# Kernel optimization log

Hardware: AMD Instinct MI355X
Metric: run time of the kernel (lower is better)

The kernel has to match this reference:

```python
import jax, jax.numpy as jnp
import numpy as np

HS, NH, HD = 768, 12, 64
MLP_DIM = 3072
WS = 14            # window size
B, H, W = 8, 64, 64
EPS = 1e-6


def _ln(x, g, b):
    mu = jnp.mean(x, axis=-1, keepdims=True)
    var = jnp.mean(jnp.square(x - mu), axis=-1, keepdims=True)
    return (x - mu) * jax.lax.rsqrt(var + EPS) * g + b


def setup_inputs() -> dict:
    key = jax.random.key(0)
    ks = jax.random.split(key, 8)
    s = 0.02
    return {
        "x": jax.random.normal(ks[0], (B, H, W, HS), dtype=jnp.float32),
        "ln1_g": jnp.ones((HS,), jnp.float32),
        "ln1_b": jnp.zeros((HS,), jnp.float32),
        "qkv_w": jax.random.normal(ks[1], (HS, 3 * HS), jnp.float32) * s,
        "qkv_b": jnp.zeros((3 * HS,), jnp.float32),
        "proj_w": jax.random.normal(ks[2], (HS, HS), jnp.float32) * s,
        "proj_b": jnp.zeros((HS,), jnp.float32),
        "rel_pos_h": jax.random.normal(ks[3], (2 * WS - 1, HD), jnp.float32) * s,
        "rel_pos_w": jax.random.normal(ks[4], (2 * WS - 1, HD), jnp.float32) * s,
        "ln2_g": jnp.ones((HS,), jnp.float32),
        "ln2_b": jnp.zeros((HS,), jnp.float32),
        "mlp_w1": jax.random.normal(ks[5], (HS, MLP_DIM), jnp.float32) * s,
        "mlp_b1": jnp.zeros((MLP_DIM,), jnp.float32),
        "mlp_w2": jax.random.normal(ks[6], (MLP_DIM, HS), jnp.float32) * s,
        "mlp_b2": jnp.zeros((HS,), jnp.float32),
    }


def reference(x, ln1_g, ln1_b, qkv_w, qkv_b, proj_w, proj_b,
              rel_pos_h, rel_pos_w, ln2_g, ln2_b,
              mlp_w1, mlp_b1, mlp_w2, mlp_b2):
    b, h, w, c = x.shape
    shortcut = x
    y = _ln(x, ln1_g, ln1_b)

    # ---- window partition (pad H,W to multiple of WS) ----
    pad = (-h) % WS
    hp = h + pad
    y = jnp.pad(y, ((0, 0), (0, pad), (0, pad), (0, 0)))
    n = hp // WS  # windows per side
    y = y.reshape(b, n, WS, n, WS, c).transpose(0, 1, 3, 2, 4, 5)
    y = y.reshape(b * n * n, WS, WS, c)          # (Bw, 14, 14, C)
    bw = y.shape[0]
    tok = WS * WS                                 # 196

    # ---- attention with decomposed relative position bias ----
    qkv = y.reshape(bw, tok, c) @ qkv_w + qkv_b   # (Bw, 196, 3C)
    qkv = qkv.reshape(bw, tok, 3, NH, HD).transpose(2, 0, 3, 1, 4)
    qkv = qkv.reshape(3, bw * NH, tok, HD)
    q, k, v = qkv[0], qkv[1], qkv[2]
    scale = HD ** -0.5
    attn = jnp.einsum('bqd,bkd->bqk', q * scale, k)  # (Bw*NH, 196, 196)

    idx = jnp.arange(WS)[:, None] - jnp.arange(WS)[None, :] + (WS - 1)
    Rh = rel_pos_h[idx]                            # (14, 14, HD)
    Rw = rel_pos_w[idx]                            # (14, 14, HD)
    qr = q.reshape(bw * NH, WS, WS, HD)
    rel_h = jnp.einsum('bhwc,hkc->bhwk', qr, Rh)   # (Bnh, h, w, k_h)
    rel_w = jnp.einsum('bhwc,wkc->bhwk', qr, Rw)   # (Bnh, h, w, k_w)
    bias = (rel_h[:, :, :, :, None] + rel_w[:, :, :, None, :])
    attn = attn + bias.reshape(bw * NH, tok, tok)

    attn = jax.nn.softmax(attn, axis=-1)
    out = jnp.einsum('bqk,bkd->bqd', attn, v)      # (Bw*NH, 196, HD)
    out = out.reshape(bw, NH, WS, WS, HD).transpose(0, 2, 3, 1, 4)
    out = out.reshape(bw, WS, WS, c) @ proj_w + proj_b

    # ---- window unpartition + crop ----
    out = out.reshape(b, n, n, WS, WS, c).transpose(0, 1, 3, 2, 4, 5)
    out = out.reshape(b, hp, hp, c)[:, :h, :w, :]

    x = shortcut + out

    # ---- MLP block ----
    y2 = _ln(x, ln2_g, ln2_b)
    y2 = jax.nn.gelu(y2 @ mlp_w1 + mlp_b1, approximate=False) @ mlp_w2 + mlp_b2
    return x + y2
```

## Files before the change

### kernel.cpp

```cpp
#include <hip/hip_runtime.h>
#include <hip/hip_bf16.h>
#include <math.h>


#define HS 768
#define NHEADS 12
#define HD 64
#define WSZ 14
#define TOK 196
#define HWDIM 64
#define NSIDE 5
#define WIN_PER_B 25

typedef __attribute__((ext_vector_type(8))) short short8;
typedef __attribute__((ext_vector_type(4))) float floatx4;
typedef __attribute__((ext_vector_type(4))) unsigned short ushort4v;

__device__ __forceinline__ float bf2f(unsigned short u) {
    union { unsigned int i; float f; } w; w.i = ((unsigned int)u) << 16; return w.f;
}
__device__ __forceinline__ unsigned short f2bu(float f) {
    __hip_bfloat16 h = __float2bfloat16(f);
    return *(unsigned short*)&h;
}

__device__ __forceinline__ void gload16(const void* g, void* l) {
    __builtin_amdgcn_global_load_lds(
        (const __attribute__((address_space(1))) void*)g,
        (__attribute__((address_space(3))) void*)l, 16, 0, 0);
}

__device__ __forceinline__ int gather_src(int m, int M, int win_base) {
    if (m >= M) return -1;
    int lwin = m / TOK, tok = m - lwin * TOK;
    int win = win_base + lwin;
    int bb = win / WIN_PER_B, r = win - bb * WIN_PER_B;
    int wi = r / NSIDE, wj = r - wi * NSIDE;
    int ti = tok / WSZ, tj = tok - ti * WSZ;
    int h = wi * WSZ + ti, w = wj * WSZ + tj;
    if (h < HWDIM && w < HWDIM) return (bb * HWDIM + h) * HWDIM + w;
    return -1;
}

__global__ __launch_bounds__(256)
void cvt_t_k(const float* __restrict__ src, __hip_bfloat16* __restrict__ dst,
             int K, int N) {
    __shared__ float t[32][33];
    int n0 = blockIdx.x * 32, k0 = blockIdx.y * 32;
    int tc = threadIdx.x & 31, tr8 = threadIdx.x >> 5;
    #pragma unroll
    for (int i = 0; i < 4; ++i) {
        int r = tr8 + i * 8;
        t[r][tc] = src[(size_t)(k0 + r) * N + n0 + tc];
    }
    __syncthreads();
    #pragma unroll
    for (int i = 0; i < 4; ++i) {
        int r = tr8 + i * 8;
        dst[(size_t)(n0 + r) * K + k0 + tc] = __float2bfloat16(t[tc][r]);
    }
}

__global__ __launch_bounds__(256)
void ln_k(const float* __restrict__ x, const float* __restrict__ g,
          const float* __restrict__ b, __hip_bfloat16* __restrict__ y) {
    int wave = threadIdx.x >> 6, lane = threadIdx.x & 63;
    int row = blockIdx.x * 4 + wave;
    const float4* xr = (const float4*)(x + (size_t)row * HS);
    float4 a0 = xr[lane], a1 = xr[lane + 64], a2 = xr[lane + 128];
    float s = a0.x + a0.y + a0.z + a0.w + a1.x + a1.y + a1.z + a1.w
            + a2.x + a2.y + a2.z + a2.w;
    float q = a0.x*a0.x + a0.y*a0.y + a0.z*a0.z + a0.w*a0.w
            + a1.x*a1.x + a1.y*a1.y + a1.z*a1.z + a1.w*a1.w
            + a2.x*a2.x + a2.y*a2.y + a2.z*a2.z + a2.w*a2.w;
    #pragma unroll
    for (int off = 32; off > 0; off >>= 1) {
        s += __shfl_down(s, off, 64);
        q += __shfl_down(q, off, 64);
    }
    s = __shfl(s, 0, 64);
    q = __shfl(q, 0, 64);
    float mu = s * (1.0f / HS);
    float var = q * (1.0f / HS) - mu * mu;
    float rstd = rsqrtf(var + 1e-6f);
    const float4* g4 = (const float4*)g;
    const float4* b4 = (const float4*)b;
    unsigned short* yr = (unsigned short*)y + (size_t)row * HS;
    float4 av[3] = {a0, a1, a2};
    #pragma unroll
    for (int c = 0; c < 3; ++c) {
        float4 gv = g4[lane + 64 * c], bv = b4[lane + 64 * c];
        float4 a = av[c];
        ushort4v o;
        o[0] = f2bu((a.x - mu) * rstd * gv.x + bv.x);
        o[1] = f2bu((a.y - mu) * rstd * gv.y + bv.y);
        o[2] = f2bu((a.z - mu) * rstd * gv.z + bv.z);
        o[3] = f2bu((a.w - mu) * rstd * gv.w + bv.w);
        *(ushort4v*)&yr[(lane + 64 * c) * 4] = o;
    }
}

template<int EP, int AGATHER, int BM, int BN, int KSPLIT, int XSWZ = 0, int RING = 3>
__global__ __launch_bounds__(256, 4)
void gemm_k(const __hip_bfloat16* __restrict__ A,
            const __hip_bfloat16* __restrict__ Bt,
            const float* __restrict__ bias,
            int M, int N, int K,
            __hip_bfloat16* __restrict__ oq, __hip_bfloat16* __restrict__ okk,
            __hip_bfloat16* __restrict__ ov,
            float* __restrict__ of, const float* __restrict__ resid,
            __hip_bfloat16* __restrict__ oh,
            int win_base, int m_base)
{
    constexpr int LPW = (BM + BN) / 64;
    constexpr int FI = BM / 32;
    constexpr int FJ = BN / 32;
    constexpr int ASZ = BM * 32;
    constexpr int BSZ = BN * 32;
    __shared__ __align__(16) unsigned short lds[RING * (ASZ + BSZ)];
    unsigned short* Asb = lds;
    unsigned short* Bsb = lds + RING * ASZ;

    int tid = threadIdx.x;
    int wave = tid >> 6, lane = tid & 63;
    int n16 = lane & 15, quad = lane >> 4;
    int wrr = wave >> 1, wcc = wave & 1;

    int bx = blockIdx.x, by = blockIdx.y;
    if constexpr (XSWZ) {
        int gx = gridDim.x, gy = gridDim.y;
        int lin = by * gx + bx;
        int nwg = gx * gy;
        int qq = nwg >> 3, rr8 = nwg & 7;
        int xcd = lin & 7, pos = lin >> 3;
        int swz = (xcd < rr8) ? (xcd * (qq + 1) + pos)
                              : (rr8 * (qq + 1) + (xcd - rr8) * qq + pos);
        bx = swz % gx;
        by = swz / gx;
    }
    int bm = by * BM;
    int bn = bx * BN;
    int kz = (KSPLIT > 1) ? blockIdx.z : 0;
    int kseg = K / KSPLIT;

    int srow = tid >> 2;
    int q4 = tid & 3;
    int skoff = (q4 ^ ((srow >> 1) & 3)) << 3;

    const unsigned short* Au = (const unsigned short*)A;
    const unsigned short* Bu = (const unsigned short*)Bt;

    int src0 = 0, src1 = 0;
    if (AGATHER) {
        int s0 = gather_src(bm + srow, M, win_base);
        src0 = s0 >= 0 ? s0 : 0;
        if (BM == 128) {
            int s1 = gather_src(bm + 64 + srow, M, win_base);
            src1 = s1 >= 0 ? s1 : 0;
        }
    } else {
        int m0 = bm + srow;
        src0 = m0 < M ? m0 : 0;
        if (BM == 128) { int m1 = bm + 64 + srow; src1 = m1 < M ? m1 : 0; }
    }

    const unsigned short* ap0 = Au + (size_t)src0 * K + kz * kseg + skoff;
    const unsigned short* ap1 = Au + (size_t)src1 * K + kz * kseg + skoff;
    const unsigned short* bp0 = Bu + (size_t)(bn + srow) * K + kz * kseg + skoff;
    const unsigned short* bp1 = Bu + (size_t)(bn + 64 + srow) * K + kz * kseg + skoff;

    auto stage = [&](int kt, int b) {
        size_t ko = (size_t)kt * 32;
        gload16(ap0 + ko, Asb + b * ASZ + wave * 512);
        if constexpr (BM == 128) gload16(ap1 + ko, Asb + b * ASZ + 2048 + wave * 512);
        gload16(bp0 + ko, Bsb + b * BSZ + wave * 512);
        if constexpr (BN == 128) gload16(bp1 + ko, Bsb + b * BSZ + 2048 + wave * 512);
    };

    floatx4 acc[FI][FJ] = {};
    int xr = (n16 >> 1) & 3;
    int nt = kseg >> 5;

    stage(0, 0);
    if (nt > 1) stage(1, 1);
    if (RING > 3 && nt > 2) stage(2, 2);

    int cur = 0;
    for (int t = 0; t < nt; ++t) {
        int ahead = nt - 1 - t;
        if (RING >= 4 && ahead >= 2) {
            if constexpr (LPW == 4)      asm volatile("s_waitcnt vmcnt(8)" ::: "memory");
            else if constexpr (LPW == 3) asm volatile("s_waitcnt vmcnt(6)" ::: "memory");
            else                         asm volatile("s_waitcnt vmcnt(4)" ::: "memory");
        } else if (ahead >= 1) {
            if constexpr (LPW == 4)      asm volatile("s_waitcnt vmcnt(4)" ::: "memory");
            else if constexpr (LPW == 3) asm volatile("s_waitcnt vmcnt(3)" ::: "memory");
            else                         asm volatile("s_waitcnt vmcnt(2)" ::: "memory");
        } else {
            asm volatile("s_waitcnt vmcnt(0)" ::: "memory");
        }
        __builtin_amdgcn_s_barrier();
        if (t + RING - 1 < nt) {
            int nb = cur + RING - 1; if (nb >= RING) nb -= RING;
            stage(t + RING - 1, nb);
        }
        short8 af[FI], bf[FJ];
        #pragma unroll
        for (int i = 0; i < FI; ++i) {
            int ra = wrr * (BM / 2) + i * 16 + n16;
            af[i] = *(const short8*)&Asb[cur * ASZ + ra * 32 + ((quad ^ xr) << 3)];
        }
        #pragma unroll
        for (int j = 0; j < FJ; ++j) {
            int rb = wcc * (BN / 2) + j * 16 + n16;
            bf[j] = *(const short8*)&Bsb[cur * BSZ + rb * 32 + ((quad ^ xr) << 3)];
        }
        #pragma unroll
        for (int i = 0; i < FI; ++i)
            #pragma unroll
            for (int j = 0; j < FJ; ++j)
                acc[i][j] = __builtin_amdgcn_mfma_f32_16x16x32_bf16(
                    af[i], bf[j], acc[i][j], 0, 0, 0);
        asm volatile("s_waitcnt lgkmcnt(0)" ::: "memory");
        cur += 1; if (cur >= RING) cur -= RING;
    }

    int rbase = bm + wrr * (BM / 2) + quad * 4;
    int cbase = bn + wcc * (BN / 2) + n16;

    if constexpr (EP == 0 || EP == 2) {
        constexpr int CLD = BN + 8;
        __syncthreads();
        unsigned short* Cs = lds;
        int ruseW[FI * 4];
        if (EP == 0) {
            #pragma unroll
            for (int i = 0; i < FI; ++i)
                #pragma unroll
                for (int r = 0; r < 4; ++r)
                    ruseW[i * 4 + r] = gather_src(rbase + i * 16 + r, M, win_base) >= 0;
        }
        #pragma unroll
        for (int j = 0; j < FJ; ++j) {
            int col_l = wcc * (BN / 2) + j * 16 + n16;
            float bcol = bias[bn + col_l];
            #pragma unroll
            for (int i = 0; i < FI; ++i) {
                #pragma unroll
                for (int r = 0; r < 4; ++r) {
                    int row_l = wrr * (BM / 2) + i * 16 + quad * 4 + r;
                    float val = acc[i][j][r] + bcol;
                    float vv;
                    if (EP == 0) {
                        vv = ruseW[i * 4 + r] ? val : bcol;
                    } else {
                        vv = 0.5f * val * (1.0f + erff(val * 0.70710678118654752f));
                    }
                    Cs[row_l * CLD + col_l] = f2bu(vv);
                }
            }
        }
        __syncthreads();
        #pragma unroll
        for (int rep = 0; rep < (BM * (BN / 64)) / 256; ++rep) {
            int idx = rep * 256 + tid;
            int row_l = idx / (BN / 64);
            int half = idx - row_l * (BN / 64);
            int m = bm + row_l;
            if (m < M) {
                unsigned short* srcu = &Cs[row_l * CLD + half * 64];
                unsigned short* dstu;
                if (EP == 0) {
                    int lwin = m / TOK, tok = m - lwin * TOK;
                    int colg = bn + half * 64;
                    int which = colg / HS;
                    int head = (colg - which * HS) >> 6;
                    __hip_bfloat16* dstp = (which == 0) ? oq : ((which == 1) ? okk : ov);
                    dstu = (unsigned short*)dstp +
                           ((size_t)(lwin * NHEADS + head) * TOK + tok) * HD;
                } else {
                    dstu = (unsigned short*)oh + (size_t)m * N + bn + half * 64;
                }
                #pragma unroll
                for (int s = 0; s < 8; ++s)
                    *(uint4*)(dstu + s * 8) = *(const uint4*)(srcu + s * 8);
            }
        }
    } else {
        int rowoff[FI * 4];
        int ruse[FI * 4];
        #pragma unroll
        for (int i = 0; i < FI; ++i) {
            #pragma unroll
            for (int r = 0; r < 4; ++r) {
                int ii = i * 4 + r;
                int row = rbase + i * 16 + r;
                if (EP == 1) {
                    int lwin = row / TOK, tok = row - lwin * TOK;
                    int win = win_base + lwin;
                    int bb = win / WIN_PER_B, rr2 = win - bb * WIN_PER_B;
                    int wi = rr2 / NSIDE, wj = rr2 - wi * NSIDE;
                    int ti = tok / WSZ, tj = tok - ti * WSZ;
                    int h = wi * WSZ + ti, w = wj * WSZ + tj;
                    ruse[ii] = (h < HWDIM) && (w < HWDIM);
                    rowoff[ii] = ((bb * HWDIM + h) * HWDIM + w) * HS;
                } else {
                    rowoff[ii] = (m_base + row) * HS;
                    ruse[ii] = 1;
                }
            }
        }
        #pragma unroll
        for (int j = 0; j < FJ; ++j) {
            int col = cbase + j * 16;
            float bcol = bias[col];
            if (EP == 3 && KSPLIT > 1 && kz != 0) bcol = 0.0f;
            #pragma unroll
            for (int i = 0; i < FI; ++i) {
                #pragma unroll
                for (int r = 0; r < 4; ++r) {
                    int ii = i * 4 + r;
                    int row = rbase + i * 16 + r;
                    if (row >= M) continue;
                    float val = acc[i][j][r] + bcol;
                    if (EP == 1) {
                        if (ruse[ii]) {
                            size_t idx = (size_t)rowoff[ii] + col;
                            of[idx] = resid[idx] + val;
                        }
                    } else {
                        size_t idx = (size_t)rowoff[ii] + col;
                        if (KSPLIT > 1) {
                            unsafeAtomicAdd(&of[idx], val);
                        } else {
                            of[idx] += val;
                        }
                    }
                }
            }
        }
    }
}

__global__ __launch_bounds__(256)
void attn_k(const __hip_bfloat16* __restrict__ qb, const __hip_bfloat16* __restrict__ kb,
            const __hip_bfloat16* __restrict__ vb,
            const float* __restrict__ rph, const float* __restrict__ rpw,
            __hip_bfloat16* __restrict__ ao)
{
    __shared__ __align__(16) unsigned short lds[40736];
    unsigned short* Ks = lds;
    unsigned short* Vt = lds + 14112;
    unsigned short* KE = lds + 28960;
    unsigned short* scr = lds + 37280;

    int bid = blockIdx.x;
    int lwin = bid / NHEADS, head = bid - lwin * NHEADS;
    size_t base = (size_t)(lwin * NHEADS + head) * TOK * HD;
    const unsigned short* q = (const unsigned short*)qb + base;
    const unsigned short* k = (const unsigned short*)kb + base;
    const unsigned short* v = (const unsigned short*)vb + base;

    int tid = threadIdx.x;
    int wave = tid >> 6, lane = tid & 63;
    int n16 = lane & 15, quad = lane >> 4;

    short8 btab[4][2];
    #pragma unroll
    for (int nt = 0; nt < 4; ++nt) {
        int n = nt * 16 + n16;
        #pragma unroll
        for (int kh = 0; kh < 2; ++kh) {
            short8 f = {0, 0, 0, 0, 0, 0, 0, 0};
            if (n < 54) {
                const float* src = (n < 27) ? (rph + (size_t)n * HD)
                                            : (rpw + (size_t)(n - 27) * HD);
                const float4* s4 = (const float4*)(src + kh * 32 + quad * 8);
                float4 a = s4[0], b = s4[1];
                f[0] = (short)f2bu(a.x * 8.0f); f[1] = (short)f2bu(a.y * 8.0f);
                f[2] = (short)f2bu(a.z * 8.0f); f[3] = (short)f2bu(a.w * 8.0f);
                f[4] = (short)f2bu(b.x * 8.0f); f[5] = (short)f2bu(b.y * 8.0f);
                f[6] = (short)f2bu(b.z * 8.0f); f[7] = (short)f2bu(b.w * 8.0f);
            }
            btab[nt][kh] = f;
        }
    }

    for (int idx = tid; idx < 1568; idx += 256) {
        int row = idx >> 3, q8 = (idx & 7) << 3;
        *(uint4*)&Ks[row * 72 + q8] = *(const uint4*)(k + (size_t)row * HD + q8);
    }
    for (int s = tid; s < 1568; s += 256) {
        int row = s >> 3, d8 = (s & 7) << 3;
        uint4 vv = *(const uint4*)(v + (size_t)row * HD + d8);
        const unsigned short* p = (const unsigned short*)&vv;
        #pragma unroll
        for (int e = 0; e < 8; ++e)
            Vt[(d8 + e) * 232 + row] = p[e];
    }
    for (int s = tid; s < 64 * 9; s += 256) {
        int r = s / 9, c = 196 + (s - r * 9) * 4;
        uint2 z = {0u, 0u};
        *(uint2*)&Vt[r * 232 + c] = z;
    }
    for (int krow = tid; krow < 208; krow += 256) {
        int ki = krow / WSZ, kj = krow - ki * WSZ;
        int valid = krow < TOK;
        #pragma unroll
        for (int c = 0; c < 32; ++c) {
            unsigned short vv = 0;
            if (valid && (c == ki || c == 14 + kj)) vv = 0x3F80;
            KE[krow * 40 + c] = vv;
        }
    }
    __syncthreads();

    unsigned short* myscr = &scr[wave * 864];
    int rl0 = quad * 4;

    for (int qt = wave; qt < 13; qt += 4) {
        int qrow = qt * 16 + n16;
        int qr = qrow < 196 ? qrow : 195;

        short8 raw0 = *(const short8*)(q + (size_t)qr * HD + quad * 8);
        short8 raw1 = *(const short8*)(q + (size_t)qr * HD + 32 + quad * 8);
        short8 qf0, qf1;
        #pragma unroll
        for (int e = 0; e < 8; ++e) {
            qf0[e] = (short)f2bu(bf2f((unsigned short)raw0[e]) * 0.125f);
            qf1[e] = (short)f2bu(bf2f((unsigned short)raw1[e]) * 0.125f);
        }

        #pragma unroll
        for (int nt = 0; nt < 4; ++nt) {
            floatx4 cr = {0.f, 0.f, 0.f, 0.f};
            cr = __builtin_amdgcn_mfma_f32_16x16x32_bf16(qf0, btab[nt][0], cr, 0, 0, 0);
            cr = __builtin_amdgcn_mfma_f32_16x16x32_bf16(qf1, btab[nt][1], cr, 0, 0, 0);
            int c = nt * 16 + n16;
            if (c < 54) {
                #pragma unroll
                for (int r = 0; r < 4; ++r)
                    myscr[(rl0 + r) * 54 + c] = f2bu(cr[r]);
            }
        }

        int ti_l = qr / WSZ, tj_l = qr - ti_l * WSZ;
        short8 qf2;
        #pragma unroll
        for (int e = 0; e < 8; ++e) {
            int d = quad * 8 + e;
            int idx_i = n16 * 54 + ti_l + 13 - d;
            int idx_j = n16 * 54 + 40 + tj_l - (d - 14);
            int idx = (d < 14) ? idx_i : idx_j;
            unsigned short vv = (d < 28) ? myscr[idx] : (unsigned short)0;
            qf2[e] = (short)vv;
        }

        floatx4 S[13];
        __builtin_amdgcn_s_setprio(1);
        #pragma unroll
        for (int nt = 0; nt < 13; ++nt) {
            int kr = nt * 16 + n16;
            short8 kf0 = *(const short8*)&Ks[kr * 72 + quad * 8];
            short8 kf1 = *(const short8*)&Ks[kr * 72 + 32 + quad * 8];
            short8 kf2 = *(const short8*)&KE[kr * 40 + quad * 8];
            floatx4 a = {0.f, 0.f, 0.f, 0.f};
            a = __builtin_amdgcn_mfma_f32_16x16x32_bf16(qf0, kf0, a, 0, 0, 0);
            a = __builtin_amdgcn_mfma_f32_16x16x32_bf16(qf1, kf1, a, 0, 0, 0);
            a = __builtin_amdgcn_mfma_f32_16x16x32_bf16(qf2, kf2, a, 0, 0, 0);
            S[nt] = a;
        }
        __builtin_amdgcn_s_setprio(0);

        if (n16 >= 4) {
            #pragma unroll
            for (int r = 0; r < 4; ++r) S[12][r] = -1e30f;
        }

        float mxr[4] = {-3e30f, -3e30f, -3e30f, -3e30f};
        #pragma unroll
        for (int nt = 0; nt < 13; ++nt)
            #pragma unroll
            for (int r = 0; r < 4; ++r) mxr[r] = fmaxf(mxr[r], S[nt][r]);
        #pragma unroll
        for (int m = 1; m <= 8; m <<= 1)
            #pragma unroll
            for (int r = 0; r < 4; ++r) mxr[r] = fmaxf(mxr[r], __shfl_xor(mxr[r], m, 64));
        float sum[4] = {0.f, 0.f, 0.f, 0.f};
        #pragma unroll
        for (int nt = 0; nt < 13; ++nt)
            #pragma unroll
            for (int r = 0; r < 4; ++r) {
                float e = __expf(S[nt][r] - mxr[r]);
                S[nt][r] = e;
                sum[r] += e;
            }
        #pragma unroll
        for (int m = 1; m <= 8; m <<= 1)
            #pragma unroll
            for (int r = 0; r < 4; ++r) sum[r] += __shfl_xor(sum[r], m, 64);
        float inv[4];
        #pragma unroll
        for (int r = 0; r < 4; ++r) inv[r] = 1.0f / sum[r];

        floatx4 O[4] = {{0.f,0.f,0.f,0.f},{0.f,0.f,0.f,0.f},{0.f,0.f,0.f,0.f},{0.f,0.f,0.f,0.f}};
        __builtin_amdgcn_s_setprio(1);
        #pragma unroll
        for (int ks = 0; ks < 7; ++ks) {
            #pragma unroll
            for (int r = 0; r < 4; ++r) {
                myscr[(rl0 + r) * 40 + n16] = f2bu(S[2 * ks][r] * inv[r]);
                myscr[(rl0 + r) * 40 + 16 + n16] =
                    (2 * ks + 1 < 13) ? f2bu(S[2 * ks + 1][r] * inv[r]) : (unsigned short)0;
            }
            short8 pf = *(const short8*)&myscr[n16 * 40 + quad * 8];
            #pragma unroll
            for (int nt4 = 0; nt4 < 4; ++nt4) {
                short8 vf = *(const short8*)&Vt[(nt4 * 16 + n16) * 232 + ks * 32 + quad * 8];
                O[nt4] = __builtin_amdgcn_mfma_f32_16x16x32_bf16(pf, vf, O[nt4], 0, 0, 0);
            }
        }
        __builtin_amdgcn_s_setprio(0);

        #pragma unroll
        for (int nt4 = 0; nt4 < 4; ++nt4) {
            int d = nt4 * 16 + n16;
            #pragma unroll
            for (int r = 0; r < 4; ++r) {
                int row = qt * 16 + rl0 + r;
                if (row < 196) {
                    ao[((size_t)(lwin * TOK + row)) * HS + head * HD + d] =
                        __float2bfloat16(O[nt4][r]);
                }
            }
        }
    }
}

extern "C" void kernel_launch(void* const* d_in, const int* in_sizes, int n_in,
                              void* d_out, int out_size, void* d_ws, size_t ws_size,
                              hipStream_t stream)
{
    const float* x      = (const float*)d_in[0];
    const float* ln1_g  = (const float*)d_in[1];
    const float* ln1_b  = (const float*)d_in[2];
    const float* qkv_w  = (const float*)d_in[3];
    const float* qkv_b  = (const float*)d_in[4];
    const float* proj_w = (const float*)d_in[5];
    const float* proj_b = (const float*)d_in[6];
    const float* rph    = (const float*)d_in[7];
    const float* rpw    = (const float*)d_in[8];
    const float* ln2_g  = (const float*)d_in[9];
    const float* ln2_b  = (const float*)d_in[10];
    const float* mlp_w1 = (const float*)d_in[11];
    const float* mlp_b1 = (const float*)d_in[12];
    const float* mlp_w2 = (const float*)d_in[13];
    const float* mlp_b2 = (const float*)d_in[14];
    float* out = (float*)d_out;

    char* ws = (char*)d_ws;
    __hip_bfloat16* wqkv  = (__hip_bfloat16*)(ws + 0);
    __hip_bfloat16* wproj = (__hip_bfloat16*)(ws + 3538944);
    __hip_bfloat16* wm1   = (__hip_bfloat16*)(ws + 4718592);
    __hip_bfloat16* wm2   = (__hip_bfloat16*)(ws + 9437184);
    __hip_bfloat16* ybuf  = (__hip_bfloat16*)(ws + 14155776);
    char* R2 = ws + 64487424;
    __hip_bfloat16* hid = (__hip_bfloat16*)(R2);

    const size_t PERWIN = 301056;
    int nwin_chunk, nchunks;
    if (ws_size >= 64487424ull + 4ull * 200 * PERWIN) {
        nwin_chunk = 200; nchunks = 1;
    } else if (ws_size >= 64487424ull + 4ull * 100 * PERWIN) {
        nwin_chunk = 100; nchunks = 2;
    } else {
        nwin_chunk = 25; nchunks = 8;
    }
    size_t bufsz = (size_t)nwin_chunk * PERWIN;
    __hip_bfloat16* qc = (__hip_bfloat16*)(R2);
    __hip_bfloat16* kc = (__hip_bfloat16*)(R2 + bufsz);
    __hip_bfloat16* vc = (__hip_bfloat16*)(R2 + 2 * bufsz);
    __hip_bfloat16* ao = (__hip_bfloat16*)(R2 + 3 * bufsz);

    int mlpch, nmlp;
    if (ws_size >= 64487424ull + (size_t)16384 * 3072 * 2) {
        mlpch = 16384; nmlp = 2;
    } else {
        mlpch = 8192; nmlp = 4;
    }

    cvt_t_k<<<dim3(72, 24), 256, 0, stream>>>(qkv_w,  wqkv,  768, 2304);
    cvt_t_k<<<dim3(24, 24), 256, 0, stream>>>(proj_w, wproj, 768, 768);
    cvt_t_k<<<dim3(96, 24), 256, 0, stream>>>(mlp_w1, wm1,   768, 3072);
    cvt_t_k<<<dim3(24, 96), 256, 0, stream>>>(mlp_w2, wm2,  3072, 768);

    ln_k<<<dim3(8192), 256, 0, stream>>>(x, ln1_g, ln1_b, ybuf);

    for (int c = 0; c < nchunks; ++c) {
        int M = nwin_chunk * TOK;
        int wb = c * nwin_chunk;
        gemm_k<0, 1, 128, 128, 1, 1, 3><<<dim3(18, (M + 127) / 128), 256, 0, stream>>>(
            ybuf, wqkv, qkv_b, M, 2304, 768,
            qc, kc, vc, nullptr, nullptr, nullptr, wb, 0);
        attn_k<<<dim3(nwin_chunk * NHEADS), 256, 0, stream>>>(
            qc, kc, vc, rph, rpw, ao);
        gemm_k<1, 0, 128, 128, 1, 1, 3><<<dim3(6, (M + 127) / 128), 256, 0, stream>>>(
            ao, wproj, proj_b, M, 768, 768,
            nullptr, nullptr, nullptr, out, x, nullptr, wb, 0);
    }

    ln_k<<<dim3(8192), 256, 0, stream>>>(out, ln2_g, ln2_b, ybuf);

    for (int mc = 0; mc < nmlp; ++mc) {
        gemm_k<2, 0, 128, 128, 1, 1, 3><<<dim3(24, mlpch / 128), 256, 0, stream>>>(
            ybuf + (size_t)mc * mlpch * HS, wm1, mlp_b1, mlpch, 3072, 768,
            nullptr, nullptr, nullptr, nullptr, nullptr, hid, 0, 0);
        gemm_k<3, 0, 128, 64, 1, 1, 3><<<dim3(12, mlpch / 128), 256, 0, stream>>>(
            hid, wm2, mlp_b2, mlpch, 768, 3072,
            nullptr, nullptr, nullptr, out, nullptr, nullptr, 0, mc * mlpch);
    }
}
```

Before: 1.309 ms.

## Add 256x256-tile 8-wave GEMM with XCD swizzle for MLP up-projection

Adds a dedicated GEMM kernel for the first MLP layer (bias + exact GELU) that uses 256x256 output tiles, 512 threads and 128KB of dynamic LDS. Global loads for the next K-slice are interleaved with MFMA work on the current slice, and the workgroup order is remapped so neighbouring tiles land on the same XCD. The goal is more operand reuse per tile and better L2 locality than the generic 128x128 kernel. In exchange it runs one workgroup per CU, holds a large register accumulator, and stages the epilogue through LDS.

```diff
diff --git a/kernel.cpp b/kernel.cpp
--- a/kernel.cpp
+++ b/kernel.cpp
@@ -342,6 +342,143 @@
     }
 }
 
+template<int XSWZ>
+__global__ __launch_bounds__(512, 1)
+void gemm8p_k(const __hip_bfloat16* __restrict__ A,
+              const __hip_bfloat16* __restrict__ Bt,
+              const float* __restrict__ bias,
+              int M, int N, int K,
+              __hip_bfloat16* __restrict__ oh)
+{
+    extern __shared__ unsigned short dl[];
+
+    int tid = threadIdx.x;
+    int w = tid >> 6, l = tid & 63;
+    int n16 = l & 15, quad = l >> 4;
+    int wrr = w >> 2, wcc = w & 3;
+
+    int bx = blockIdx.x, by = blockIdx.y;
+    if constexpr (XSWZ) {
+        int gx = gridDim.x, gy = gridDim.y;
+        int lin = by * gx + bx;
+        int nwg = gx * gy;
+        int qq = nwg >> 3, rr8 = nwg & 7;
+        int xcd = lin & 7, pos = lin >> 3;
+        int swz = (xcd < rr8) ? (xcd * (qq + 1) + pos)
+                              : (rr8 * (qq + 1) + (xcd - rr8) * qq + pos);
+        bx = swz % gx;
+        by = swz / gx;
+    }
+    int bm = by * 256, bn = bx * 256;
+
+    int srow_l = tid >> 3;
+    int sg = (tid & 7) ^ (srow_l & 7);
+    const unsigned short* Au = (const unsigned short*)A;
+    const unsigned short* Bu = (const unsigned short*)Bt;
+    const unsigned short* apA[2][2];
+    const unsigned short* apB[2][2];
+    #pragma unroll
+    for (int h = 0; h < 2; ++h)
+        #pragma unroll
+        for (int e = 0; e < 2; ++e) {
+            apA[h][e] = Au + (size_t)(bm + h * 128 + e * 64 + srow_l) * K + sg * 8;
+            apB[h][e] = Bu + (size_t)(bn + h * 128 + e * 64 + srow_l) * K + sg * 8;
+        }
+
+    auto stage_half = [&](int t, int hs, int d) {
+        int op = hs >> 1, h = hs & 1;
+        size_t ko = (size_t)t * 64;
+        const unsigned short* s0 = (op ? apB[h][0] : apA[h][0]) + ko;
+        const unsigned short* s1 = (op ? apB[h][1] : apA[h][1]) + ko;
+        unsigned short* dst = dl + d * 32768 + op * 16384 + (h * 128 + w * 8) * 64;
+        gload16(s0, dst);
+        gload16(s1, dst + 4096);
+    };
+
+    floatx4 acc[8][4] = {};
+    int xr7 = n16 & 7;
+    int nt = K >> 6;
+
+    stage_half(0, 0, 0); stage_half(0, 1, 0);
+    stage_half(0, 2, 0); stage_half(0, 3, 0);
+    asm volatile("s_waitcnt vmcnt(0)" ::: "memory");
+    __builtin_amdgcn_s_barrier();
+
+    for (int t = 0; t < nt; ++t) {
+        int d = t & 1;
+        int stg = (t + 1 < nt);
+        const unsigned short* Ab = dl + d * 32768;
+        const unsigned short* Bb = dl + d * 32768 + 16384;
+
+        short8 bfr[4][2];
+        #pragma unroll
+        for (int j = 0; j < 4; ++j) {
+            int rb = wcc * 64 + j * 16 + n16;
+            #pragma unroll
+            for (int ks = 0; ks < 2; ++ks)
+                bfr[j][ks] = *(const short8*)&Bb[rb * 64 + (((ks * 4 + quad)) ^ xr7) * 8];
+        }
+
+        #pragma unroll
+        for (int q = 0; q < 4; ++q) {
+            short8 afr[2][2];
+            #pragma unroll
+            for (int ii = 0; ii < 2; ++ii) {
+                int ra = wrr * 128 + (2 * q + ii) * 16 + n16;
+                #pragma unroll
+                for (int ks = 0; ks < 2; ++ks)
+                    afr[ii][ks] = *(const short8*)&Ab[ra * 64 + (((ks * 4 + quad)) ^ xr7) * 8];
+            }
+            if (stg) stage_half(t + 1, q, d ^ 1);
+            __builtin_amdgcn_s_setprio(1);
+            #pragma unroll
+            for (int ks = 0; ks < 2; ++ks)
+                #pragma unroll
+                for (int ii = 0; ii < 2; ++ii)
+                    #pragma unroll
+                    for (int j = 0; j < 4; ++j)
+                        acc[2 * q + ii][j] = __builtin_amdgcn_mfma_f32_16x16x32_bf16(
+                            afr[ii][ks], bfr[j][ks], acc[2 * q + ii][j], 0, 0, 0);
+            __builtin_amdgcn_s_setprio(0);
+        }
+        asm volatile("s_waitcnt vmcnt(0) lgkmcnt(0)" ::: "memory");
+        __builtin_amdgcn_s_barrier();
+    }
+
+    unsigned short* Cs = dl;
+    float bcol[4];
+    #pragma unroll
+    for (int j = 0; j < 4; ++j)
+        bcol[j] = bias[bn + wcc * 64 + j * 16 + n16];
+    #pragma unroll
+    for (int h = 0; h < 2; ++h) {
+        if (wrr == h) {
+            #pragma unroll
+            for (int i = 0; i < 8; ++i)
+                #pragma unroll
+                for (int j = 0; j < 4; ++j) {
+                    int col_l = wcc * 64 + j * 16 + n16;
+                    #pragma unroll
+                    for (int r = 0; r < 4; ++r) {
+                        int row_l = i * 16 + quad * 4 + r;
+                        float val = acc[i][j][r] + bcol[j];
+                        float ge = 0.5f * val * (1.0f + erff(val * 0.70710678118654752f));
+                        Cs[row_l * 264 + col_l] = f2bu(ge);
+                    }
+                }
+        }
+        __syncthreads();
+        int row_l = tid >> 2, seg = tid & 3;
+        unsigned short* dstu = (unsigned short*)oh +
+            (size_t)(bm + h * 128 + row_l) * N + bn + seg * 64;
+        const unsigned short* srcu = &Cs[row_l * 264 + seg * 64];
+        #pragma unroll
+        for (int s = 0; s < 8; ++s)
+            *(uint4*)(dstu + s * 8) = *(const uint4*)(srcu + s * 8);
+        __syncthreads();
+    }
+}
+
 __global__ __launch_bounds__(256)
 void attn_k(const __hip_bfloat16* __restrict__ qb, const __hip_bfloat16* __restrict__ kb,
             const __hip_bfloat16* __restrict__ vb,
@@ -589,6 +726,13 @@
         mlpch = 8192; nmlp = 4;
     }
 
+    static int init8p = 0;
+    if (!init8p) {
+        hipFuncSetAttribute((const void*)gemm8p_k<1>,
+                            hipFuncAttributeMaxDynamicSharedMemorySize, 131072);
+        init8p = 1;
+    }
+
     cvt_t_k<<<dim3(72, 24), 256, 0, stream>>>(qkv_w,  wqkv,  768, 2304);
     cvt_t_k<<<dim3(24, 24), 256, 0, stream>>>(proj_w, wproj, 768, 768);
     cvt_t_k<<<dim3(96, 24), 256, 0, stream>>>(mlp_w1, wm1,   768, 3072);
@@ -612,9 +756,8 @@
     ln_k<<<dim3(8192), 256, 0, stream>>>(out, ln2_g, ln2_b, ybuf);
 
     for (int mc = 0; mc < nmlp; ++mc) {
-        gemm_k<2, 0, 128, 128, 1, 1, 3><<<dim3(24, mlpch / 128), 256, 0, stream>>>(
-            ybuf + (size_t)mc * mlpch * HS, wm1, mlp_b1, mlpch, 3072, 768,
-            nullptr, nullptr, nullptr, nullptr, nullptr, hid, 0, 0);
+        gemm8p_k<1><<<dim3(12, mlpch / 256), 512, 131072, stream>>>(
+            ybuf + (size_t)mc * mlpch * HS, wm1, mlp_b1, mlpch, 3072, 768, hid);
         gemm_k<3, 0, 128, 64, 1, 1, 3><<<dim3(12, mlpch / 128), 256, 0, stream>>>(
             hid, wm2, mlp_b2, mlpch, 768, 3072,
             nullptr, nullptr, nullptr, out, nullptr, nullptr, 0, mc * mlpch);
```

After: 1.377 ms. +5.2%, slower.
